# Kernel tuning notes

Measured on AMD Instinct MI355X. Metric: run time of the kernel, lower is better.

The kernel has to match this reference:

```python
import jax, jax.numpy as jnp
import numpy as np

# Each of the 16 real-valued binary logic ops is a polynomial
#   c0 + c1*a + c2*b + c3*a*b
# Rows correspond to op_idx 0..15 from bin_op().
_OP_COEFFS = np.array([
    [0.,  0.,  0.,  0.],   # 0: false
    [0.,  0.,  0.,  1.],   # 1: a*b
    [0.,  1.,  0., -1.],   # 2: a*(1-b)
    [0.,  1.,  0.,  0.],   # 3: a
    [0.,  0.,  1., -1.],   # 4: (1-a)*b
    [0.,  0.,  1.,  0.],   # 5: b
    [0.,  1.,  1., -2.],   # 6: xor
    [0.,  1.,  1., -1.],   # 7: or
    [1., -1., -1.,  1.],   # 8: nor
    [1., -1., -1.,  2.],   # 9: xnor
    [1.,  0., -1.,  0.],   # 10: not b
    [1.,  0., -1.,  1.],   # 11: b -> a
    [1., -1.,  0.,  0.],   # 12: not a
    [1., -1.,  0.,  1.],   # 13: a -> b
    [1.,  0.,  0., -1.],   # 14: nand
    [1.,  0.,  0.,  0.],   # 15: true
], dtype=np.float32)

BATCH, IN_DIM, OUT_DIM = 2048, 16384, 16384


def setup_inputs() -> dict:
    key = jax.random.key(0)
    k1, k2, k3, k4 = jax.random.split(key, 4)
    x = jax.random.uniform(k1, (BATCH, IN_DIM), dtype=jnp.float32)
    idx_a = jax.random.randint(k2, (OUT_DIM,), 0, IN_DIM, dtype=jnp.int32)
    idx_b = jax.random.randint(k3, (OUT_DIM,), 0, IN_DIM, dtype=jnp.int32)
    weights = jax.random.normal(k4, (OUT_DIM, 16), dtype=jnp.float32)
    return {"x": x, "idx_a": idx_a, "idx_b": idx_b, "weights": weights}


def reference(x, idx_a, idx_b, weights):
    # gate probabilities over the 16 ops, per output neuron: [out_dim, 16]
    probs = jax.nn.softmax(weights, axis=-1)
    # collapse the 16-way weighted combination into 4 polynomial coeffs
    coef = probs @ jnp.asarray(_OP_COEFFS, dtype=probs.dtype)  # [out_dim, 4]
    a = x[:, idx_a]  # [batch, out_dim]
    b = x[:, idx_b]  # [batch, out_dim]
    out = coef[:, 0] + coef[:, 1] * a + coef[:, 2] * b + coef[:, 3] * (a * b)
    return out
```

## Files before the change

### kernel.cpp

```cpp
#include <hip/hip_runtime.h>
#include <hip/hip_fp16.h>

#define IN_DIM  16384
#define OUT_DIM 16384
#define BATCH   2048
#define TPB     512
#define ITS     (OUT_DIM / (TPB * 4))
#define CHK     (IN_DIM / (TPB * 8))

typedef float f32x4 __attribute__((ext_vector_type(4)));

struct h2x2 { __half2 ab, cd; };

__device__ __constant__ float OPC[16][4] = {
    {0.f, 0.f, 0.f, 0.f}, {0.f, 0.f, 0.f, 1.f}, {0.f, 1.f, 0.f, -1.f}, {0.f, 1.f, 0.f, 0.f},
    {0.f, 0.f, 1.f, -1.f}, {0.f, 0.f, 1.f, 0.f}, {0.f, 1.f, 1.f, -2.f}, {0.f, 1.f, 1.f, -1.f},
    {1.f, -1.f, -1.f, 1.f}, {1.f, -1.f, -1.f, 2.f}, {1.f, 0.f, -1.f, 0.f}, {1.f, 0.f, -1.f, 1.f},
    {1.f, -1.f, 0.f, 0.f}, {1.f, -1.f, 0.f, 1.f}, {1.f, 0.f, 0.f, -1.f}, {1.f, 0.f, 0.f, 0.f}};

__global__ __launch_bounds__(256) void prep_kernel(const float* __restrict__ w,
                                                   const int* __restrict__ ia,
                                                   const int* __restrict__ ib,
                                                   h2x2* __restrict__ coefh,
                                                   unsigned* __restrict__ packed) {
    int j = blockIdx.x * 256 + threadIdx.x;
    if (j >= OUT_DIM) return;

    const float4* wr = (const float4*)(w + (size_t)j * 16);
    float wv[16];
    float4 w0 = wr[0], w1 = wr[1], w2 = wr[2], w3 = wr[3];
    wv[0] = w0.x; wv[1] = w0.y; wv[2] = w0.z; wv[3] = w0.w;
    wv[4] = w1.x; wv[5] = w1.y; wv[6] = w1.z; wv[7] = w1.w;
    wv[8] = w2.x; wv[9] = w2.y; wv[10] = w2.z; wv[11] = w2.w;
    wv[12] = w3.x; wv[13] = w3.y; wv[14] = w3.z; wv[15] = w3.w;

    float m = wv[0];
#pragma unroll
    for (int k = 1; k < 16; ++k) m = fmaxf(m, wv[k]);
    float s = 0.f;
#pragma unroll
    for (int k = 0; k < 16; ++k) { wv[k] = expf(wv[k] - m); s += wv[k]; }
    float inv = 1.f / s;

    float c0 = 0.f, c1 = 0.f, c2 = 0.f, c3 = 0.f;
#pragma unroll
    for (int k = 0; k < 16; ++k) {
        float p = wv[k];
        c0 = fmaf(p, OPC[k][0], c0);
        c1 = fmaf(p, OPC[k][1], c1);
        c2 = fmaf(p, OPC[k][2], c2);
        c3 = fmaf(p, OPC[k][3], c3);
    }
    h2x2 c;
    c.ab = __floats2half2_rn(c0 * inv, c1 * inv);
    c.cd = __floats2half2_rn(c2 * inv, c3 * inv);
    coefh[j] = c;
    packed[j] = ((unsigned)ia[j] << 1) | ((unsigned)ib[j] << 17);
}

__device__ __forceinline__ unsigned pack2(float a, float b) {
    return __builtin_bit_cast(unsigned, __builtin_amdgcn_cvt_pkrtz(a, b));
}

__global__ __launch_bounds__(TPB, 4) void logic_kernel(const float* __restrict__ x,
                                                       const unsigned* __restrict__ packed,
                                                       const h2x2* __restrict__ coefh,
                                                       float* __restrict__ out) {
    __shared__ __half lds[IN_DIM];

    const int tid = threadIdx.x;
    const size_t row = blockIdx.x;

    {
        const float4* s4 = (const float4*)(x + row * IN_DIM);
        uint4 tt[CHK];
#pragma unroll
        for (int c = 0; c < CHK; ++c) {
            float4 v0 = s4[(c * TPB + tid) * 2 + 0];
            float4 v1 = s4[(c * TPB + tid) * 2 + 1];
            tt[c].x = pack2(v0.x, v0.y); tt[c].y = pack2(v0.z, v0.w);
            tt[c].z = pack2(v1.x, v1.y); tt[c].w = pack2(v1.z, v1.w);
        }
#pragma unroll
        for (int c = 0; c < CHK; ++c)
            *(uint4*)((char*)lds + (size_t)(c * TPB + tid) * 16) = tt[c];
    }

    uint4 pi = *(const uint4*)(packed + tid * 4);
    h2x2 cA = coefh[tid * 4 + 0];
    h2x2 cB = coefh[tid * 4 + 1];
    h2x2 cC = coefh[tid * 4 + 2];
    h2x2 cD = coefh[tid * 4 + 3];

    __syncthreads();

    const char* bufc = (const char*)lds;
    float* outr = out + row * IN_DIM;

#pragma unroll
    for (int it = 0; it < ITS; ++it) {
        uint4 pin = pi;
        h2x2 nA = cA, nB = cB, nC = cC, nD = cD;
        if (it + 1 < ITS) {
            const int jn = ((it + 1) * TPB + tid) * 4;
            pin = *(const uint4*)(packed + jn);
            nA = coefh[jn + 0];
            nB = coefh[jn + 1];
            nC = coefh[jn + 2];
            nD = coefh[jn + 3];
        }
        __builtin_amdgcn_sched_barrier(0);

        const int j0 = (it * TPB + tid) * 4;
        f32x4 o;
#define COL(P, CF, FLD)                                                             \
        {                                                                           \
            float a = __half2float(*(const __half*)(bufc + ((P) & 0xFFFFu)));       \
            float b = __half2float(*(const __half*)(bufc + ((P) >> 16)));           \
            float c0 = __low2float(CF.ab), c1 = __high2float(CF.ab);                \
            float c2 = __low2float(CF.cd), c3 = __high2float(CF.cd);                \
            o.FLD = fmaf(a, fmaf(c3, b, c1), fmaf(c2, b, c0));                      \
        }
        COL(pi.x, cA, x)
        COL(pi.y, cB, y)
        COL(pi.z, cC, z)
        COL(pi.w, cD, w)
#undef COL
        *(f32x4*)(outr + j0) = o;

        pi = pin; cA = nA; cB = nB; cC = nC; cD = nD;
    }
}

extern "C" void kernel_launch(void* const* d_in, const int* in_sizes, int n_in,
                              void* d_out, int out_size, void* d_ws, size_t ws_size,
                              hipStream_t stream) {
    const float* x = (const float*)d_in[0];
    const int* ia = (const int*)d_in[1];
    const int* ib = (const int*)d_in[2];
    const float* w = (const float*)d_in[3];
    float* out = (float*)d_out;

    h2x2* coefh = (h2x2*)d_ws;
    unsigned* packed = (unsigned*)((char*)d_ws + (size_t)OUT_DIM * sizeof(h2x2));

    prep_kernel<<<OUT_DIM / 256, 256, 0, stream>>>(w, ia, ib, coefh, packed);
    logic_kernel<<<BATCH, TPB, 0, stream>>>(x, packed, coefh, out);
}
```

Baseline: 55.75 us.

## Process two batch rows per block with interleaved half2 LDS layout

Each block now handles two batch rows, storing their fp16 values interleaved as half2 pairs in a 64KB LDS buffer. One gather load per index then fetches both rows' values, and the index and coefficient loads are shared across the two rows. Packed indices are shifted by one more bit to match the 4-byte stride. The trade-off is twice the LDS per block and a lower occupancy target in launch_bounds (2 instead of 4), which gives fewer resident blocks to hide global memory latency.

```diff
diff --git a/kernel.cpp b/kernel.cpp
--- a/kernel.cpp
+++ b/kernel.cpp
@@ -5,6 +5,7 @@
 #define OUT_DIM 16384
 #define BATCH   2048
 #define TPB     512
+#define NBLK    (BATCH / 2)
 #define ITS     (OUT_DIM / (TPB * 4))
 #define CHK     (IN_DIM / (TPB * 8))
 
@@ -55,35 +56,48 @@
     c.ab = __floats2half2_rn(c0 * inv, c1 * inv);
     c.cd = __floats2half2_rn(c2 * inv, c3 * inv);
     coefh[j] = c;
-    packed[j] = ((unsigned)ia[j] << 1) | ((unsigned)ib[j] << 17);
+    packed[j] = ((unsigned)ia[j] << 2) | ((unsigned)ib[j] << 18);
 }
 
 __device__ __forceinline__ unsigned pack2(float a, float b) {
     return __builtin_bit_cast(unsigned, __builtin_amdgcn_cvt_pkrtz(a, b));
 }
 
-__global__ __launch_bounds__(TPB, 4) void logic_kernel(const float* __restrict__ x,
+__global__ __launch_bounds__(TPB, 2) void logic_kernel(const float* __restrict__ x,
                                                        const unsigned* __restrict__ packed,
                                                        const h2x2* __restrict__ coefh,
                                                        float* __restrict__ out) {
-    __shared__ __half lds[IN_DIM];
+    __shared__ __half lds[2 * IN_DIM];
 
     const int tid = threadIdx.x;
-    const size_t row = blockIdx.x;
+    const size_t rowA = (size_t)blockIdx.x * 2;
 
     {
-        const float4* s4 = (const float4*)(x + row * IN_DIM);
-        uint4 tt[CHK];
+        const float4* sA = (const float4*)(x + rowA * IN_DIM);
+        const float4* sB = (const float4*)(x + (rowA + 1) * IN_DIM);
+        float4 vA[2 * CHK], vB[2 * CHK];
 #pragma unroll
         for (int c = 0; c < CHK; ++c) {
-            float4 v0 = s4[(c * TPB + tid) * 2 + 0];
-            float4 v1 = s4[(c * TPB + tid) * 2 + 1];
-            tt[c].x = pack2(v0.x, v0.y); tt[c].y = pack2(v0.z, v0.w);
-            tt[c].z = pack2(v1.x, v1.y); tt[c].w = pack2(v1.z, v1.w);
+            vA[2 * c + 0] = sA[(c * TPB + tid) * 2 + 0];
+            vA[2 * c + 1] = sA[(c * TPB + tid) * 2 + 1];
+            vB[2 * c + 0] = sB[(c * TPB + tid) * 2 + 0];
+            vB[2 * c + 1] = sB[(c * TPB + tid) * 2 + 1];
         }
 #pragma unroll
-        for (int c = 0; c < CHK; ++c)
-            *(uint4*)((char*)lds + (size_t)(c * TPB + tid) * 16) = tt[c];
+        for (int c = 0; c < CHK; ++c) {
+            const size_t e = (size_t)(c * TPB + tid) * 8;
+            uint4 t0, t1;
+            t0.x = pack2(vA[2 * c].x, vB[2 * c].x);
+            t0.y = pack2(vA[2 * c].y, vB[2 * c].y);
+            t0.z = pack2(vA[2 * c].z, vB[2 * c].z);
+            t0.w = pack2(vA[2 * c].w, vB[2 * c].w);
+            t1.x = pack2(vA[2 * c + 1].x, vB[2 * c + 1].x);
+            t1.y = pack2(vA[2 * c + 1].y, vB[2 * c + 1].y);
+            t1.z = pack2(vA[2 * c + 1].z, vB[2 * c + 1].z);
+            t1.w = pack2(vA[2 * c + 1].w, vB[2 * c + 1].w);
+            *(uint4*)((char*)lds + e * 4) = t0;
+            *(uint4*)((char*)lds + e * 4 + 16) = t1;
+        }
     }
 
     uint4 pi = *(const uint4*)(packed + tid * 4);
@@ -95,7 +109,8 @@
     __syncthreads();
 
     const char* bufc = (const char*)lds;
-    float* outr = out + row * IN_DIM;
+    float* outrA = out + rowA * IN_DIM;
+    float* outrB = outrA + IN_DIM;
 
 #pragma unroll
     for (int it = 0; it < ITS; ++it) {
@@ -112,21 +127,25 @@
         __builtin_amdgcn_sched_barrier(0);
 
         const int j0 = (it * TPB + tid) * 4;
-        f32x4 o;
-#define COL(P, CF, FLD)                                                             \
-        {                                                                           \
-            float a = __half2float(*(const __half*)(bufc + ((P) & 0xFFFFu)));       \
-            float b = __half2float(*(const __half*)(bufc + ((P) >> 16)));           \
-            float c0 = __low2float(CF.ab), c1 = __high2float(CF.ab);                \
-            float c2 = __low2float(CF.cd), c3 = __high2float(CF.cd);                \
-            o.FLD = fmaf(a, fmaf(c3, b, c1), fmaf(c2, b, c0));                      \
+        f32x4 oA, oB;
+#define COL(P, CF, FLD)                                                              \
+        {                                                                            \
+            __half2 ap = *(const __half2*)(bufc + ((P) & 0xFFFFu));                  \
+            __half2 bp = *(const __half2*)(bufc + ((P) >> 16));                      \
+            float aA = __low2float(ap), aB = __high2float(ap);                       \
+            float bA = __low2float(bp), bB = __high2float(bp);                       \
+            float c0 = __low2float(CF.ab), c1 = __high2float(CF.ab);                 \
+            float c2 = __low2float(CF.cd), c3 = __high2float(CF.cd);                 \
+            oA.FLD = fmaf(aA, fmaf(c3, bA, c1), fmaf(c2, bA, c0));                   \
+            oB.FLD = fmaf(aB, fmaf(c3, bB, c1), fmaf(c2, bB, c0));                   \
         }
         COL(pi.x, cA, x)
         COL(pi.y, cB, y)
         COL(pi.z, cC, z)
         COL(pi.w, cD, w)
 #undef COL
-        *(f32x4*)(outr + j0) = o;
+        *(f32x4*)(outrA + j0) = oA;
+        *(f32x4*)(outrB + j0) = oB;
 
         pi = pin; cA = nA; cB = nB; cC = nC; cD = nD;
     }
@@ -145,5 +164,5 @@
     unsigned* packed = (unsigned*)((char*)d_ws + (size_t)OUT_DIM * sizeof(h2x2));
 
     prep_kernel<<<OUT_DIM / 256, 256, 0, stream>>>(w, ia, ib, coefh, packed);
-    logic_kernel<<<BATCH, TPB, 0, stream>>>(x, packed, coefh, out);
+    logic_kernel<<<NBLK, TPB, 0, stream>>>(x, packed, coefh, out);
 }
```

Result: no change. 56.72 us (+1.7%).
